# Optimization experiments

Hardware: AMD Instinct MI355X
Metric: run time of the kernel (lower is better)

Reference implementation:

```python
import jax, jax.numpy as jnp
import numpy as np

T = 3          # num_node_type
B = 8          # batch
N = 512        # max_doc_len
F_IN = 256     # in_features
F_OUT = 128    # out_features
NE = 10        # num_edge_type (embedding has NE+1 rows, row 0 = padding)
ALPHA = 0.2    # leaky relu slope
NEG = -9e15    # masked-score fill, same constant as torch source


def setup_inputs() -> dict:
    key = jax.random.key(0)
    ks = jax.random.split(key, 7)
    node_rep = jax.random.normal(ks[0], (B, N, F_IN), jnp.float32)
    node_type_mask_rep = jax.random.uniform(ks[1], (T, B, N, 1), jnp.float32)
    adj = jax.random.randint(ks[2], (B, N, N), 0, NE + 1, jnp.int32)
    W = jax.random.normal(ks[3], (T, F_IN, F_OUT), jnp.float32) * 0.05
    b = jnp.zeros((T, F_OUT), jnp.float32)
    # attention vector a in R^{2F} split into halves (GAT trick): a([h_i, x2_ij]) = h_i.a1 + x2_ij.a2 + a_b
    a1 = jax.random.normal(ks[4], (F_OUT,), jnp.float32) * 0.05
    a2 = jax.random.normal(ks[5], (F_OUT,), jnp.float32) * 0.05
    a_b = jnp.zeros((), jnp.float32)
    emb = jax.random.normal(ks[6], (NE + 1, F_OUT), jnp.float32) * 0.05
    emb = emb.at[0].set(0.0)  # padding_idx=0
    return {"node_rep": node_rep, "node_type_mask_rep": node_type_mask_rep,
            "adj": adj, "W": W, "b": b, "a1": a1, "a2": a2, "a_b": a_b, "emb": emb}


def reference(node_rep, node_type_mask_rep, adj, W, b, a1, a2, a_b, emb):
    # typed projection: h = sum_t (node_rep @ W_t + b_t) * mask_t   -> (B, N, F_OUT)
    h = jnp.sum((jnp.einsum('bni,tio->tbno', node_rep, W) + b[:, None, None, :])
                * node_type_mask_rep, axis=0)
    # edge-type embeddings: (B, N, N, F_OUT)
    E = emb[adj]
    # x_2[b,i,j] = h[b,j] + E[b,i,j]
    x2 = h[:, None, :, :] + E
    # score[b,i,j] = leakyrelu(a1.h_i + a2.x2_ij + a_b)  (decomposed concat-linear)
    s = (jnp.einsum('bif,f->bi', h, a1)[:, :, None]
         + jnp.einsum('bijf,f->bij', x2, a2) + a_b)
    s = jnp.where(s > 0, s, ALPHA * s)
    s = jnp.where(adj > 0, s, jnp.float32(NEG))
    attn = jax.nn.softmax(s, axis=2)
    # weighted sum over neighbors of x_2 (NOT h), then ELU
    out = jnp.einsum('bij,bijf->bif', attn, x2)
    return jax.nn.elu(out)
```

## Files before the change

kernel.cpp:

```cpp
#include <hip/hip_runtime.h>

constexpr int kB    = 8;
constexpr int kN    = 512;
constexpr int kFIN  = 256;
constexpr int kFOUT = 128;
constexpr int kNE   = 10;
constexpr int kBN   = kB * kN;
constexpr float kALPHA = 0.2f;
constexpr float kNEG   = -9e15f;

__global__ __launch_bounds__(128) void proj_kernel(
    const float* __restrict__ node_rep,
    const float* __restrict__ mask,
    const float* __restrict__ W,
    float* __restrict__ part)
{
    __shared__ float xs[8][64];
    __shared__ float pcomb[3][8][kFOUT];

    const int tid  = threadIdx.x;
    const int rb   = blockIdx.x >> 2;
    const int sl   = blockIdx.x & 3;
    const int row0 = rb * 8;
    const int k0   = sl * 64;

    {
        const int r = tid >> 4, q = tid & 15;
        *(float4*)&xs[r][q * 4] =
            *(const float4*)&node_rep[(size_t)(row0 + r) * kFIN + k0 + q * 4];
    }
    __syncthreads();

    const int o0 = (tid & 63) * 2;
    const int kh = tid >> 6;

    float2 acc[3][8];
    #pragma unroll
    for (int t = 0; t < 3; ++t)
        #pragma unroll
        for (int r = 0; r < 8; ++r) acc[t][r] = {0.f, 0.f};

    const float* Wo = W + o0;

    #pragma unroll
    for (int c = 0; c < 8; ++c) {
        const int kb = kh * 32 + c * 4;
        float2 w[3][4];
        #pragma unroll
        for (int t = 0; t < 3; ++t)
            #pragma unroll
            for (int cc = 0; cc < 4; ++cc)
                w[t][cc] = *(const float2*)&Wo[(size_t)(t * kFIN + k0 + kb + cc) * kFOUT];
        float4 xv[8];
        #pragma unroll
        for (int r = 0; r < 8; ++r)
            xv[r] = *(const float4*)&xs[r][kb];
        #pragma unroll
        for (int cc = 0; cc < 4; ++cc)
            #pragma unroll
            for (int r = 0; r < 8; ++r) {
                const float x = ((const float*)&xv[r])[cc];
                acc[0][r].x = fmaf(w[0][cc].x, x, acc[0][r].x);
                acc[0][r].y = fmaf(w[0][cc].y, x, acc[0][r].y);
                acc[1][r].x = fmaf(w[1][cc].x, x, acc[1][r].x);
                acc[1][r].y = fmaf(w[1][cc].y, x, acc[1][r].y);
                acc[2][r].x = fmaf(w[2][cc].x, x, acc[2][r].x);
                acc[2][r].y = fmaf(w[2][cc].y, x, acc[2][r].y);
            }
    }

    if (kh == 1) {
        #pragma unroll
        for (int t = 0; t < 3; ++t)
            #pragma unroll
            for (int r = 0; r < 8; ++r)
                *(float2*)&pcomb[t][r][o0] = acc[t][r];
    }
    __syncthreads();

    if (kh == 0) {
        #pragma unroll
        for (int r = 0; r < 8; ++r) {
            const int row = row0 + r;
            const float m0 = mask[0 * kBN + row];
            const float m1 = mask[1 * kBN + row];
            const float m2 = mask[2 * kBN + row];
            float2 pv;
            pv.x = m0 * (acc[0][r].x + pcomb[0][r][o0])
                 + m1 * (acc[1][r].x + pcomb[1][r][o0])
                 + m2 * (acc[2][r].x + pcomb[2][r][o0]);
            pv.y = m0 * (acc[0][r].y + pcomb[0][r][o0 + 1])
                 + m1 * (acc[1][r].y + pcomb[1][r][o0 + 1])
                 + m2 * (acc[2][r].y + pcomb[2][r][o0 + 1]);
            *(float2*)&part[((size_t)sl * kBN + row) * kFOUT + o0] = pv;
        }
    }
}

__global__ __launch_bounds__(256) void reduce_kernel(
    const float* __restrict__ part,
    const float* __restrict__ mask,
    const float* __restrict__ bias,
    const float* __restrict__ a1,
    const float* __restrict__ a2,
    const float* __restrict__ a_b,
    const float* __restrict__ emb,
    float* __restrict__ h,
    float* __restrict__ s1,
    float* __restrict__ s2,
    float* __restrict__ emb_a2)
{
    __shared__ float hls[8][kFOUT];

    const int tid  = threadIdx.x;
    const int row0 = blockIdx.x * 8;
    const int o    = tid & 127;
    const int rh   = tid >> 7;

    #pragma unroll
    for (int rr = 0; rr < 4; ++rr) {
        const int r   = rh * 4 + rr;
        const int row = row0 + r;
        float hv = part[((size_t)0 * kBN + row) * kFOUT + o]
                 + part[((size_t)1 * kBN + row) * kFOUT + o]
                 + part[((size_t)2 * kBN + row) * kFOUT + o]
                 + part[((size_t)3 * kBN + row) * kFOUT + o];
        hv += mask[0 * kBN + row] * bias[0 * kFOUT + o]
            + mask[1 * kBN + row] * bias[1 * kFOUT + o]
            + mask[2 * kBN + row] * bias[2 * kFOUT + o];
        h[(size_t)row * kFOUT + o] = hv;
        hls[r][o] = hv;
    }
    __syncthreads();

    {
        const int wv = tid >> 6, lane = tid & 63;
        #pragma unroll
        for (int rr = 0; rr < 2; ++rr) {
            const int r = wv * 2 + rr;
            const float v0 = hls[r][lane];
            const float v1 = hls[r][64 + lane];
            float p1 = v0 * a1[lane] + v1 * a1[64 + lane];
            float p2 = v0 * a2[lane] + v1 * a2[64 + lane];
            #pragma unroll
            for (int off = 32; off; off >>= 1) {
                p1 += __shfl_down(p1, off);
                p2 += __shfl_down(p2, off);
            }
            if (lane == 0) {
                s1[row0 + r] = p1 + a_b[0];
                s2[row0 + r] = p2;
            }
        }
    }

    if (blockIdx.x == 0 && tid < 176) {
        const int e = tid >> 4, l = tid & 15;
        float p = 0.f;
        #pragma unroll
        for (int k8 = 0; k8 < 8; ++k8)
            p += emb[e * kFOUT + l + k8 * 16] * a2[l + k8 * 16];
        #pragma unroll
        for (int off = 8; off; off >>= 1) p += __shfl_xor(p, off);
        if (l == 0) emb_a2[e] = p;
    }
}

__global__ __launch_bounds__(512) void attn_kernel(
    const int*   __restrict__ adj,
    const float* __restrict__ emb,
    const float* __restrict__ h,
    const float* __restrict__ s1,
    const float* __restrict__ s2,
    const float* __restrict__ emb_a2g,
    float* __restrict__ out)
{
    __shared__ float sc[8][kN + 4];
    __shared__ int   adjs[8][kN];
    __shared__ float scT[kN][8];
    __shared__ float wsum[8][16];
    __shared__ float ea2[16];

    const int tid = threadIdx.x;
    const int b   = blockIdx.x >> 6;
    const int i0  = (blockIdx.x & 63) * 8;

    if (tid < 16) ea2[tid] = emb_a2g[tid];
    __syncthreads();

    const int*   adjb = adj + ((size_t)(b * kN + i0)) * kN;
    const float* s2b  = s2 + b * kN;
    #pragma unroll
    for (int it = 0; it < 2; ++it) {
        const int idx = tid + it * 512;
        const int r = idx >> 7, jq = idx & 127;
        const int4   av  = *(const int4*)&adjb[(size_t)r * kN + jq * 4];
        const float4 s2v = *(const float4*)&s2b[jq * 4];
        const float  sr  = s1[b * kN + i0 + r];
        float4 sv; float s;
        s = sr + s2v.x + ea2[av.x]; s = s > 0.f ? s : kALPHA * s; sv.x = av.x > 0 ? s : kNEG;
        s = sr + s2v.y + ea2[av.y]; s = s > 0.f ? s : kALPHA * s; sv.y = av.y > 0 ? s : kNEG;
        s = sr + s2v.z + ea2[av.z]; s = s > 0.f ? s : kALPHA * s; sv.z = av.z > 0 ? s : kNEG;
        s = sr + s2v.w + ea2[av.w]; s = s > 0.f ? s : kALPHA * s; sv.w = av.w > 0 ? s : kNEG;
        *(float4*)&sc[r][jq * 4] = sv;
        *(int4*)&adjs[r][jq * 4] = av;
    }
    __syncthreads();

    {
        const int r = tid >> 6, lane = tid & 63;
        float v[8]; int av[8];
        #pragma unroll
        for (int k = 0; k < 8; ++k) {
            v[k]  = sc[r][lane + k * 64];
            av[k] = adjs[r][lane + k * 64];
        }
        float m = v[0];
        #pragma unroll
        for (int k = 1; k < 8; ++k) m = fmaxf(m, v[k]);
        #pragma unroll
        for (int off = 32; off; off >>= 1) m = fmaxf(m, __shfl_xor(m, off));
        float sum = 0.f;
        #pragma unroll
        for (int k = 0; k < 8; ++k) { v[k] = __expf(v[k] - m); sum += v[k]; }
        #pragma unroll
        for (int off = 32; off; off >>= 1) sum += __shfl_xor(sum, off);
        const float inv = 1.0f / sum;
        #pragma unroll
        for (int k = 0; k < 8; ++k) {
            v[k] *= inv;
            scT[lane + k * 64][r] = v[k];
        }
        #pragma unroll
        for (int e = 1; e <= kNE; ++e) {
            float p = 0.f;
            #pragma unroll
            for (int k = 0; k < 8; ++k) p += (av[k] == e) ? v[k] : 0.f;
            #pragma unroll
            for (int off = 32; off; off >>= 1) p += __shfl_xor(p, off);
            if (lane == 0) wsum[r][e] = p;
        }
    }
    __syncthreads();

    const int f4l = tid & 31;
    const int rg  = (tid >> 5) & 1;
    const int js  = tid >> 6;
    const float* hb  = h + ((size_t)(b * kN + js * 64)) * kFOUT + f4l * 4;
    const float* sct = &scT[js * 64][rg * 4];

    float4 acc0 = {0,0,0,0}, acc1 = {0,0,0,0}, acc2 = {0,0,0,0}, acc3 = {0,0,0,0};
    #pragma unroll 4
    for (int jj = 0; jj < 64; ++jj) {
        const float4 w4 = *(const float4*)&sct[jj * 8];
        const float4 hv = *(const float4*)&hb[(size_t)jj * kFOUT];
        acc0.x = fmaf(w4.x, hv.x, acc0.x); acc0.y = fmaf(w4.x, hv.y, acc0.y);
        acc0.z = fmaf(w4.x, hv.z, acc0.z); acc0.w = fmaf(w4.x, hv.w, acc0.w);
        acc1.x = fmaf(w4.y, hv.x, acc1.x); acc1.y = fmaf(w4.y, hv.y, acc1.y);
        acc1.z = fmaf(w4.y, hv.z, acc1.z); acc1.w = fmaf(w4.y, hv.w, acc1.w);
        acc2.x = fmaf(w4.z, hv.x, acc2.x); acc2.y = fmaf(w4.z, hv.y, acc2.y);
        acc2.z = fmaf(w4.z, hv.z, acc2.z); acc2.w = fmaf(w4.z, hv.w, acc2.w);
        acc3.x = fmaf(w4.w, hv.x, acc3.x); acc3.y = fmaf(w4.w, hv.y, acc3.y);
        acc3.z = fmaf(w4.w, hv.z, acc3.z); acc3.w = fmaf(w4.w, hv.w, acc3.w);
    }
    __syncthreads();

    float* parts_lo = (float*)adjs;
    float* parts_hi = (float*)sc;
    {
        float* pbase = (js < 4) ? parts_lo + js * 1024
                                : parts_hi + (js - 4) * 1024;
        const int rbase = rg * 4;
        *(float4*)&pbase[(rbase + 0) * kFOUT + f4l * 4] = acc0;
        *(float4*)&pbase[(rbase + 1) * kFOUT + f4l * 4] = acc1;
        *(float4*)&pbase[(rbase + 2) * kFOUT + f4l * 4] = acc2;
        *(float4*)&pbase[(rbase + 3) * kFOUT + f4l * 4] = acc3;
    }
    __syncthreads();

    if (tid < 256) {
        const int r  = tid >> 5;
        const int fl = (tid & 31) * 4;
        float4 a = {0,0,0,0};
        #pragma unroll
        for (int p = 0; p < 4; ++p) {
            const float4 v0 = *(const float4*)&parts_lo[p * 1024 + r * kFOUT + fl];
            const float4 v1 = *(const float4*)&parts_hi[p * 1024 + r * kFOUT + fl];
            a.x += v0.x + v1.x; a.y += v0.y + v1.y;
            a.z += v0.z + v1.z; a.w += v0.w + v1.w;
        }
        #pragma unroll
        for (int e = 1; e <= kNE; ++e) {
            const float  wv = wsum[r][e];
            const float4 ev = *(const float4*)&emb[e * kFOUT + fl];
            a.x = fmaf(wv, ev.x, a.x); a.y = fmaf(wv, ev.y, a.y);
            a.z = fmaf(wv, ev.z, a.z); a.w = fmaf(wv, ev.w, a.w);
        }
        a.x = a.x > 0.f ? a.x : expm1f(a.x);
        a.y = a.y > 0.f ? a.y : expm1f(a.y);
        a.z = a.z > 0.f ? a.z : expm1f(a.z);
        a.w = a.w > 0.f ? a.w : expm1f(a.w);
        *(float4*)&out[((size_t)(b * kN + i0 + r)) * kFOUT + fl] = a;
    }
}

extern "C" void kernel_launch(void* const* d_in, const int* in_sizes, int n_in,
                              void* d_out, int out_size, void* d_ws, size_t ws_size,
                              hipStream_t stream) {
    const float* node_rep = (const float*)d_in[0];
    const float* mask     = (const float*)d_in[1];
    const int*   adj      = (const int*)  d_in[2];
    const float* W        = (const float*)d_in[3];
    const float* bias     = (const float*)d_in[4];
    const float* a1       = (const float*)d_in[5];
    const float* a2       = (const float*)d_in[6];
    const float* a_b      = (const float*)d_in[7];
    const float* emb      = (const float*)d_in[8];
    float* out = (float*)d_out;

    float* ws     = (float*)d_ws;
    float* h      = ws;
    float* s1     = h + (size_t)kBN * kFOUT;
    float* s2     = s1 + kBN;
    float* emb_a2 = s2 + kBN;
    float* part   = emb_a2 + 16;

    proj_kernel<<<2048, 128, 0, stream>>>(node_rep, mask, W, part);
    reduce_kernel<<<kBN / 8, 256, 0, stream>>>(
        part, mask, bias, a1, a2, a_b, emb, h, s1, s2, emb_a2);
    attn_kernel<<<kBN / 8, 512, 0, stream>>>(
        adj, emb, h, s1, s2, emb_a2, out);
}
```

Baseline: 111.6 us.

## Use split-bf16 MFMA for typed projection with a preprocessing kernel

Replaces the FP32 FMA projection with a bf16 hi/lo split computed in a new prep kernel, followed by an MFMA 16x16x32 bf16 GEMM using three products to approximate fp32 accuracy. The per-type outputs are written to a buffer, and the reduce kernel now applies the masks and biases. This moves the GEMM onto matrix cores but adds an extra kernel launch and extra memory traffic for the converted operands, with slight precision loss from truncation.

```diff
diff --git a/kernel.cpp b/kernel.cpp
--- a/kernel.cpp
+++ b/kernel.cpp
@@ -9,96 +9,107 @@
 constexpr float kALPHA = 0.2f;
 constexpr float kNEG   = -9e15f;
 
-__global__ __launch_bounds__(128) void proj_kernel(
+typedef __attribute__((ext_vector_type(8))) short bhalf8;
+typedef __attribute__((ext_vector_type(4))) float f32x4;
+
+__device__ __forceinline__ unsigned short bf16_trunc(float x) {
+    union { float f; unsigned u; } c; c.f = x;
+    return (unsigned short)(c.u >> 16);
+}
+__device__ __forceinline__ float bf16_tof(unsigned short h) {
+    union { unsigned u; float f; } c; c.u = ((unsigned)h) << 16;
+    return c.f;
+}
+
+__global__ __launch_bounds__(256) void prep_kernel(
     const float* __restrict__ node_rep,
-    const float* __restrict__ mask,
     const float* __restrict__ W,
-    float* __restrict__ part)
+    unsigned short* __restrict__ Xh,
+    unsigned short* __restrict__ Xl,
+    unsigned short* __restrict__ Whp,
+    unsigned short* __restrict__ Wlp)
 {
-    __shared__ float xs[8][64];
-    __shared__ float pcomb[3][8][kFOUT];
-
-    const int tid  = threadIdx.x;
-    const int rb   = blockIdx.x >> 2;
-    const int sl   = blockIdx.x & 3;
-    const int row0 = rb * 8;
-    const int k0   = sl * 64;
-
-    {
-        const int r = tid >> 4, q = tid & 15;
-        *(float4*)&xs[r][q * 4] =
-            *(const float4*)&node_rep[(size_t)(row0 + r) * kFIN + k0 + q * 4];
-    }
-    __syncthreads();
-
-    const int o0 = (tid & 63) * 2;
-    const int kh = tid >> 6;
-
-    float2 acc[3][8];
+    const int tid = threadIdx.x;
+    if (blockIdx.x < 1024) {
+        const int gid  = blockIdx.x * 256 + tid;
+        const size_t base = (size_t)gid * 4;
+        const float4 v = *(const float4*)&node_rep[base];
+        ushort4 hi, lo;
+        float t;
+        hi.x = bf16_trunc(v.x); t = v.x - bf16_tof(hi.x); lo.x = bf16_trunc(t);
+        hi.y = bf16_trunc(v.y); t = v.y - bf16_tof(hi.y); lo.y = bf16_trunc(t);
+        hi.z = bf16_trunc(v.z); t = v.z - bf16_tof(hi.z); lo.z = bf16_trunc(t);
+        hi.w = bf16_trunc(v.w); t = v.w - bf16_tof(hi.w); lo.w = bf16_trunc(t);
+        *(ushort4*)&Xh[base] = hi;
+        *(ushort4*)&Xl[base] = lo;
+    } else {
+        const int g    = (blockIdx.x - 1024) * 256 + tid;
+        const int lane = g & 63;
+        const int nt   = (g >> 6) & 7;
+        const int ks   = (g >> 9) & 7;
+        const int tt   = g >> 12;
+        const int col  = nt * 16 + (lane & 15);
+        const int kb   = ks * 32 + ((lane >> 4) * 8);
+        unsigned short hbuf[8], lbuf[8];
+        #pragma unroll
+        for (int j = 0; j < 8; ++j) {
+            const float w = W[((size_t)tt * kFIN + kb + j) * kFOUT + col];
+            hbuf[j] = bf16_trunc(w);
+            lbuf[j] = bf16_trunc(w - bf16_tof(hbuf[j]));
+        }
+        const size_t dst = ((size_t)((tt * 8 + ks) * 8 + nt)) * 512 + lane * 8;
+        #pragma unroll
+        for (int j = 0; j < 8; ++j) { Whp[dst + j] = hbuf[j]; Wlp[dst + j] = lbuf[j]; }
+    }
+}
+
+__global__ __launch_bounds__(256) void proj_mfma_kernel(
+    const unsigned short* __restrict__ Xh,
+    const unsigned short* __restrict__ Xl,
+    const unsigned short* __restrict__ Whp,
+    const unsigned short* __restrict__ Wlp,
+    float* __restrict__ y)
+{
+    const int tid   = threadIdx.x;
+    const int t     = blockIdx.x % 3;
+    const int rb    = blockIdx.x / 3;
+    const int wave  = tid >> 6;
+    const int lane  = tid & 63;
+    const int wrow  = wave & 1;
+    const int whalf = wave >> 1;
+
+    const int rowA = rb * 32 + wrow * 16 + (lane & 15);
+    const unsigned short* xhp = Xh + (size_t)rowA * kFIN + ((lane >> 4) * 8);
+    const unsigned short* xlp = Xl + (size_t)rowA * kFIN + ((lane >> 4) * 8);
+
+    f32x4 acc[4] = {{0,0,0,0},{0,0,0,0},{0,0,0,0},{0,0,0,0}};
+
     #pragma unroll
-    for (int t = 0; t < 3; ++t)
-        #pragma unroll
-        for (int r = 0; r < 8; ++r) acc[t][r] = {0.f, 0.f};
-
-    const float* Wo = W + o0;
-
+    for (int ks = 0; ks < 8; ++ks) {
+        const bhalf8 Ah = *(const bhalf8*)(xhp + ks * 32);
+        const bhalf8 Al = *(const bhalf8*)(xlp + ks * 32);
+        const size_t bw = ((size_t)((t * 8 + ks) * 8 + whalf * 4)) * 512 + lane * 8;
+        #pragma unroll
+        for (int n = 0; n < 4; ++n) {
+            const bhalf8 Bh = *(const bhalf8*)(Whp + bw + n * 512);
+            const bhalf8 Bl = *(const bhalf8*)(Wlp + bw + n * 512);
+            acc[n] = __builtin_amdgcn_mfma_f32_16x16x32_bf16(Ah, Bh, acc[n], 0, 0, 0);
+            acc[n] = __builtin_amdgcn_mfma_f32_16x16x32_bf16(Ah, Bl, acc[n], 0, 0, 0);
+            acc[n] = __builtin_amdgcn_mfma_f32_16x16x32_bf16(Al, Bh, acc[n], 0, 0, 0);
+        }
+    }
+
+    const int rbase = rb * 32 + wrow * 16 + ((lane >> 4) * 4);
+    const int cbase = whalf * 64 + (lane & 15);
     #pragma unroll
-    for (int c = 0; c < 8; ++c) {
-        const int kb = kh * 32 + c * 4;
-        float2 w[3][4];
-        #pragma unroll
-        for (int t = 0; t < 3; ++t)
-            #pragma unroll
-            for (int cc = 0; cc < 4; ++cc)
-                w[t][cc] = *(const float2*)&Wo[(size_t)(t * kFIN + k0 + kb + cc) * kFOUT];
-        float4 xv[8];
-        #pragma unroll
-        for (int r = 0; r < 8; ++r)
-            xv[r] = *(const float4*)&xs[r][kb];
-        #pragma unroll
-        for (int cc = 0; cc < 4; ++cc)
-            #pragma unroll
-            for (int r = 0; r < 8; ++r) {
-                const float x = ((const float*)&xv[r])[cc];
-                acc[0][r].x = fmaf(w[0][cc].x, x, acc[0][r].x);
-                acc[0][r].y = fmaf(w[0][cc].y, x, acc[0][r].y);
-                acc[1][r].x = fmaf(w[1][cc].x, x, acc[1][r].x);
-                acc[1][r].y = fmaf(w[1][cc].y, x, acc[1][r].y);
-                acc[2][r].x = fmaf(w[2][cc].x, x, acc[2][r].x);
-                acc[2][r].y = fmaf(w[2][cc].y, x, acc[2][r].y);
-            }
-    }
-
-    if (kh == 1) {
-        #pragma unroll
-        for (int t = 0; t < 3; ++t)
-            #pragma unroll
-            for (int r = 0; r < 8; ++r)
-                *(float2*)&pcomb[t][r][o0] = acc[t][r];
-    }
-    __syncthreads();
-
-    if (kh == 0) {
-        #pragma unroll
-        for (int r = 0; r < 8; ++r) {
-            const int row = row0 + r;
-            const float m0 = mask[0 * kBN + row];
-            const float m1 = mask[1 * kBN + row];
-            const float m2 = mask[2 * kBN + row];
-            float2 pv;
-            pv.x = m0 * (acc[0][r].x + pcomb[0][r][o0])
-                 + m1 * (acc[1][r].x + pcomb[1][r][o0])
-                 + m2 * (acc[2][r].x + pcomb[2][r][o0]);
-            pv.y = m0 * (acc[0][r].y + pcomb[0][r][o0 + 1])
-                 + m1 * (acc[1][r].y + pcomb[1][r][o0 + 1])
-                 + m2 * (acc[2][r].y + pcomb[2][r][o0 + 1]);
-            *(float2*)&part[((size_t)sl * kBN + row) * kFOUT + o0] = pv;
-        }
-    }
+    for (int n = 0; n < 4; ++n)
+        #pragma unroll
+        for (int j = 0; j < 4; ++j)
+            y[((size_t)t * kBN + rbase + j) * kFOUT + cbase + n * 16] = acc[n][j];
 }
 
 __global__ __launch_bounds__(256) void reduce_kernel(
-    const float* __restrict__ part,
+    const float* __restrict__ y,
     const float* __restrict__ mask,
     const float* __restrict__ bias,
     const float* __restrict__ a1,
@@ -121,13 +132,10 @@
     for (int rr = 0; rr < 4; ++rr) {
         const int r   = rh * 4 + rr;
         const int row = row0 + r;
-        float hv = part[((size_t)0 * kBN + row) * kFOUT + o]
-                 + part[((size_t)1 * kBN + row) * kFOUT + o]
-                 + part[((size_t)2 * kBN + row) * kFOUT + o]
-                 + part[((size_t)3 * kBN + row) * kFOUT + o];
-        hv += mask[0 * kBN + row] * bias[0 * kFOUT + o]
-            + mask[1 * kBN + row] * bias[1 * kFOUT + o]
-            + mask[2 * kBN + row] * bias[2 * kFOUT + o];
+        const float hv =
+              mask[0 * kBN + row] * (y[((size_t)0 * kBN + row) * kFOUT + o] + bias[0 * kFOUT + o])
+            + mask[1 * kBN + row] * (y[((size_t)1 * kBN + row) * kFOUT + o] + bias[1 * kFOUT + o])
+            + mask[2 * kBN + row] * (y[((size_t)2 * kBN + row) * kFOUT + o] + bias[2 * kFOUT + o]);
         h[(size_t)row * kFOUT + o] = hv;
         hls[r][o] = hv;
     }
@@ -318,16 +326,21 @@
     const float* emb      = (const float*)d_in[8];
     float* out = (float*)d_out;
 
-    float* ws     = (float*)d_ws;
-    float* h      = ws;
+    float* fws    = (float*)d_ws;
+    float* h      = fws;
     float* s1     = h + (size_t)kBN * kFOUT;
     float* s2     = s1 + kBN;
     float* emb_a2 = s2 + kBN;
-    float* part   = emb_a2 + 16;
-
-    proj_kernel<<<2048, 128, 0, stream>>>(node_rep, mask, W, part);
+    float* y      = emb_a2 + 64;
+    unsigned short* Xh  = (unsigned short*)(y + (size_t)3 * kBN * kFOUT);
+    unsigned short* Xl  = Xh + (size_t)kBN * kFIN;
+    unsigned short* Whp = Xl + (size_t)kBN * kFIN;
+    unsigned short* Wlp = Whp + 3 * 8 * 8 * 512;
+
+    prep_kernel<<<1072, 256, 0, stream>>>(node_rep, W, Xh, Xl, Whp, Wlp);
+    proj_mfma_kernel<<<384, 256, 0, stream>>>(Xh, Xl, Whp, Wlp, y);
     reduce_kernel<<<kBN / 8, 256, 0, stream>>>(
-        part, mask, bias, a1, a2, a_b, emb, h, s1, s2, emb_a2);
+        y, mask, bias, a1, a2, a_b, emb, h, s1, s2, emb_a2);
     attn_kernel<<<kBN / 8, 512, 0, stream>>>(
         adj, emb, h, s1, s2, emb_a2, out);
 }
```

New measurement: 108.7 us. 1.03x faster.
